# Kernel tuning notes

Measured on AMD Instinct MI355X. Metric: run time of the kernel, lower is better.

The kernel has to match this reference:

```python
import jax, jax.numpy as jnp
import numpy as np

B, N, E = 4, 8192, 131072
NODE_F, EDGE_F, HID, ACT = 16, 1, 128, 8


def _glorot(key, shape):
    fan_in, fan_out = shape[0], shape[1]
    lim = np.sqrt(6.0 / (fan_in + fan_out))
    return jax.random.uniform(key, shape, jnp.float32, -lim, lim)


def setup_inputs() -> dict:
    key = jax.random.key(0)
    ks = jax.random.split(key, 20)
    inp = {
        'node_features': jax.random.randint(ks[0], (B, N, NODE_F), 0, 10, jnp.int32),
        'edge_index': jax.random.randint(ks[1], (B, 2, E), 0, N, jnp.int64),
        'edge_features': jax.random.normal(ks[2], (B, E, EDGE_F), jnp.float32),
        # conv1: in = 2*NODE_F + EDGE_F
        'c1_w1': _glorot(ks[3], (2 * NODE_F + EDGE_F, HID)), 'c1_b1': jnp.zeros((HID,), jnp.float32),
        'c1_w2': _glorot(ks[4], (HID, HID)), 'c1_b2': jnp.zeros((HID,), jnp.float32),
        # conv2/conv3: in = 2*HID + 1
        'c2_w1': _glorot(ks[5], (2 * HID + 1, HID)), 'c2_b1': jnp.zeros((HID,), jnp.float32),
        'c2_w2': _glorot(ks[6], (HID, HID)), 'c2_b2': jnp.zeros((HID,), jnp.float32),
        'c3_w1': _glorot(ks[7], (2 * HID + 1, HID)), 'c3_b1': jnp.zeros((HID,), jnp.float32),
        'c3_w2': _glorot(ks[8], (HID, HID)), 'c3_b2': jnp.zeros((HID,), jnp.float32),
        'lin_w': _glorot(ks[9], (NODE_F + HID, ACT)), 'lin_b': jnp.zeros((ACT,), jnp.float32),
    }
    return inp


def _edge_conv(x, src, dst, ea, w1, b1, w2, b2):
    # message: cat([x_i (target), x_j (source), edge_attr]) -> Linear -> LeakyReLU -> Linear
    m = jnp.concatenate([x[dst], x[src], ea], axis=1)          # [E, 2F+EF]
    m = jax.nn.leaky_relu(m @ w1 + b1) @ w2 + b2               # [E, out]
    out = jax.ops.segment_min(m, dst, num_segments=x.shape[0])  # min-aggregate at targets
    cnt = jnp.zeros((x.shape[0],), m.dtype).at[dst].add(1.0)
    return jnp.where(cnt[:, None] > 0, out, 0.0)                # nodes w/o in-edges -> 0 (PyG)


def _graph_fwd(x0, ei, ea, p):
    x0 = x0.astype(jnp.float32)  # torch casts to IntTensor then MLP promotes; math on integer values
    src, dst = ei[0], ei[1]      # flow='source_to_target'
    x = jax.nn.leaky_relu(_edge_conv(x0, src, dst, ea, p['c1_w1'], p['c1_b1'], p['c1_w2'], p['c1_b2']))
    x = jax.nn.leaky_relu(_edge_conv(x, src, dst, ea, p['c2_w1'], p['c2_b1'], p['c2_w2'], p['c2_b2']))
    x = jax.nn.leaky_relu(_edge_conv(x, src, dst, ea, p['c3_w1'], p['c3_b1'], p['c3_w2'], p['c3_b2']))
    x = jnp.concatenate([x0, x], axis=1)
    return jax.nn.softplus(x @ p['lin_w'] + p['lin_b'])         # [N, ACT]


def reference(node_features, edge_index, edge_features,
              c1_w1, c1_b1, c1_w2, c1_b2,
              c2_w1, c2_b1, c2_w2, c2_b2,
              c3_w1, c3_b1, c3_w2, c3_b2,
              lin_w, lin_b):
    p = dict(c1_w1=c1_w1, c1_b1=c1_b1, c1_w2=c1_w2, c1_b2=c1_b2,
             c2_w1=c2_w1, c2_b1=c2_b1, c2_w2=c2_w2, c2_b2=c2_b2,
             c3_w1=c3_w1, c3_b1=c3_b1, c3_w2=c3_w2, c3_b2=c3_b2,
             lin_w=lin_w, lin_b=lin_b)
    return jax.vmap(lambda x, ei, ea: _graph_fwd(x, ei, ea, p))(
        node_features, edge_index, edge_features)               # [B, N, ACT]
```

## Files before the change

kernel.cpp:

```cpp
#include <hip/hip_runtime.h>

#define B_ 4
#define N_ 8192
#define E_ 131072
#define HID_ 128

typedef unsigned short us8 __attribute__((ext_vector_type(8)));
typedef unsigned short us4 __attribute__((ext_vector_type(4)));
typedef unsigned int   ui4 __attribute__((ext_vector_type(4)));
typedef int            i4  __attribute__((ext_vector_type(4)));
typedef __bf16         v8bf __attribute__((ext_vector_type(8)));
typedef float          v4f  __attribute__((ext_vector_type(4)));
typedef float          v2f  __attribute__((ext_vector_type(2)));

#define KEY_INF 0xFF800000u

__device__ __forceinline__ float b2f(unsigned short u) {
    return __uint_as_float(((unsigned)u) << 16);
}
__device__ __forceinline__ unsigned short f2b(float f) {
    unsigned x = __float_as_uint(f);
    return (unsigned short)((x + 0x7fffu + ((x >> 16) & 1u)) >> 16);
}
__device__ __forceinline__ unsigned fkey(float f) {
    unsigned b = __float_as_uint(f);
    return (b & 0x80000000u) ? ~b : (b | 0x80000000u);
}
__device__ __forceinline__ float funkey(unsigned k) {
    unsigned b = (k & 0x80000000u) ? (k ^ 0x80000000u) : ~k;
    return __uint_as_float(b);
}

__global__ void k_setup(const int* __restrict__ nf, unsigned short* __restrict__ x0b,
                        unsigned* __restrict__ cnt, unsigned* __restrict__ agg) {
    const int bid = blockIdx.x, tid = threadIdx.x;
    const int gid = bid * 256 + tid;
    ui4 v = {KEY_INF, KEY_INF, KEY_INF, KEY_INF};
    ((ui4*)agg)[gid] = v;
    if (bid < 512) {
        i4 x = ((const i4*)nf)[gid];
        us4 o;
        o[0] = f2b((float)x[0]); o[1] = f2b((float)x[1]);
        o[2] = f2b((float)x[2]); o[3] = f2b((float)x[3]);
        ((us4*)x0b)[gid] = o;
    }
    if (bid < 128) cnt[gid] = 0u;
}

__global__ void k_hist(const int* __restrict__ ei, unsigned* __restrict__ cnt) {
    int gid = blockIdx.x * 256 + threadIdx.x;
    int b = gid >> 17, e = gid & (E_ - 1);
    int dst = ei[(b << 18) + E_ + e];
    atomicAdd(&cnt[(b << 13) + dst], 1u);
}

__global__ void k_scan(unsigned* __restrict__ cnt) {
    int b = blockIdx.x;
    __shared__ unsigned ps[256];
    unsigned* c = cnt + (b << 13) + threadIdx.x * 32;
    unsigned loc[32]; unsigned s = 0;
#pragma unroll
    for (int i = 0; i < 32; i++) { loc[i] = c[i]; s += loc[i]; }
    ps[threadIdx.x] = s;
    __syncthreads();
    for (int off = 1; off < 256; off <<= 1) {
        unsigned v = (threadIdx.x >= (unsigned)off) ? ps[threadIdx.x - off] : 0u;
        __syncthreads();
        ps[threadIdx.x] += v;
        __syncthreads();
    }
    unsigned run = ps[threadIdx.x] - s;
#pragma unroll
    for (int i = 0; i < 32; i++) { c[i] = run; run += loc[i]; }
}

__global__ void k_scatter(const int* __restrict__ ei, unsigned* __restrict__ wptr,
                          int* __restrict__ perm) {
    int gid = blockIdx.x * 256 + threadIdx.x;
    int b = gid >> 17, e = gid & (E_ - 1);
    int dst = ei[(b << 18) + E_ + e];
    unsigned pos = atomicAdd(&wptr[(b << 13) + dst], 1u);
    perm[(b << 17) + pos] = e;
}

__device__ __forceinline__ void repack_one(const float* __restrict__ w1, const float* __restrict__ w2,
                                           unsigned short* __restrict__ w1n, unsigned short* __restrict__ w2t,
                                           int F, int KPAD, int gid) {
    int t1 = 256 * KPAD;
    if (gid < t1) {
        int j = gid / KPAD, k = gid - j * KPAD;
        float v = 0.f;
        if (k < F) v = (j < 128) ? w1[k * 128 + j] : w1[(F + k) * 128 + (j - 128)];
        w1n[gid] = f2b(v);
    } else {
        int g = gid - t1;
        if (g < 16384) { int j = g >> 7, k = g & 127; w2t[g] = f2b(w2[k * 128 + j]); }
    }
}

__global__ void k_repack3(const float* __restrict__ w1a, const float* __restrict__ w2a,
                          const float* __restrict__ w1b, const float* __restrict__ w2b,
                          const float* __restrict__ w1c, const float* __restrict__ w2c,
                          unsigned short* __restrict__ w1n0, unsigned short* __restrict__ w2t0,
                          unsigned short* __restrict__ w1n1, unsigned short* __restrict__ w2t1,
                          unsigned short* __restrict__ w1n2, unsigned short* __restrict__ w2t2) {
    const int bid = blockIdx.x;
    const int gid = bid * 256 + threadIdx.x;
    if (bid < 96)       repack_one(w1a, w2a, w1n0, w2t0, 16, 32, gid);
    else if (bid < 288) repack_one(w1b, w2b, w1n1, w2t1, 128, 128, gid - 96 * 256);
    else                repack_one(w1c, w2c, w1n2, w2t2, 128, 128, gid - 288 * 256);
}

template<int KPAD, bool FROM_AGG>
__global__ __launch_bounds__(256, 3) void k_node(
    const unsigned short* __restrict__ xin,
    unsigned* __restrict__ agg,
    const unsigned short* __restrict__ w1n,
    const float* __restrict__ bias1,
    unsigned short* __restrict__ Yd,
    unsigned short* __restrict__ Ys)
{
    constexpr int ASTR = KPAD + 8;
    __shared__ __align__(16) unsigned short A[64 * ASTR];
    __shared__ __align__(16) unsigned short Yb[64 * 264];

    const int tid = threadIdx.x;
    const int wave = tid >> 6, lane = tid & 63, lq = lane >> 4, lm = lane & 15;
    const int tile = (blockIdx.x & 7) * 64 + (blockIdx.x >> 3);
    const int n0 = tile * 64;

    v8bf wf[4][KPAD / 32]; float b1v[4];
#pragma unroll
    for (int nt = 0; nt < 4; nt++) {
        const int col = wave * 64 + nt * 16 + lm;
#pragma unroll
        for (int ks = 0; ks < KPAD / 32; ks++)
            wf[nt][ks] = *(const v8bf*)&w1n[col * KPAD + ks * 32 + lq * 8];
        b1v[nt] = (col < 128) ? bias1[col] : 0.f;
    }

    {
        const int row = tid >> 2, p = tid & 3;
        if (FROM_AGG) {
#pragma unroll
            for (int i = 0; i < 8; i++) {
                const int c = p + 4 * i;
                unsigned* ap = agg + ((size_t)(n0 + row)) * 128 + c * 4;
                ui4 k = *(ui4*)ap;
                ui4 inf = {KEY_INF, KEY_INF, KEY_INF, KEY_INF};
                *(ui4*)ap = inf;
                us4 o;
#pragma unroll
                for (int j = 0; j < 4; j++) {
                    float v = (k[j] == KEY_INF) ? 0.f : funkey(k[j]);
                    v = (v > 0.f) ? v : 0.01f * v;
                    o[j] = f2b(v);
                }
                *(us4*)&A[row * ASTR + c * 4] = o;
            }
        } else {
            us4 v = *(const us4*)(xin + ((size_t)(n0 + row)) * 16 + p * 4);
            *(us4*)&A[row * ASTR + p * 4] = v;
            us4 z = {0, 0, 0, 0};
            *(us4*)&A[row * ASTR + 16 + p * 4] = z;
        }
    }
    __syncthreads();

#pragma unroll
    for (int mt = 0; mt < 4; mt++) {
        v4f acc[4];
#pragma unroll
        for (int nt = 0; nt < 4; nt++) acc[nt] = v4f{0.f, 0.f, 0.f, 0.f};
#pragma unroll
        for (int ks = 0; ks < KPAD / 32; ks++) {
            v8bf a = *(const v8bf*)&A[(mt * 16 + lm) * ASTR + ks * 32 + lq * 8];
#pragma unroll
            for (int nt = 0; nt < 4; nt++)
                acc[nt] = __builtin_amdgcn_mfma_f32_16x16x32_bf16(a, wf[nt][ks], acc[nt], 0, 0, 0);
        }
#pragma unroll
        for (int nt = 0; nt < 4; nt++) {
            const int col = wave * 64 + nt * 16 + lm;
#pragma unroll
            for (int r = 0; r < 4; r++)
                Yb[(mt * 16 + lq * 4 + r) * 264 + col] = f2b(acc[nt][r] + b1v[nt]);
        }
    }
    __syncthreads();

    const int bb = tile >> 7, nl0 = (tile & 127) * 64;
#pragma unroll
    for (int i = 0; i < 8; i++) {
        const int idx = tid + 256 * i;
        const int row = idx >> 5, c = idx & 31;
        us8 v = *(const us8*)&Yb[row * 264 + c * 8];
        const int col0 = c * 8;
        unsigned short* dp = (col0 < 128)
            ? (Yd + ((size_t)(bb * N_) + nl0 + row) * 128 + col0)
            : (Ys + ((size_t)(bb * N_) + nl0 + row) * 128 + (col0 - 128));
        *(us8*)dp = v;
    }
}

__global__ __launch_bounds__(256, 4) void k_edge(
    const unsigned short* __restrict__ Yd,
    const unsigned short* __restrict__ Ys,
    const int* __restrict__ ei,
    const float* __restrict__ eaf,
    const int* __restrict__ perm,
    const unsigned short* __restrict__ w2t,
    const float* __restrict__ weap,
    const float* __restrict__ bias2,
    unsigned* __restrict__ agg)
{
    __shared__ __align__(16) unsigned short Hs[128 * 136];
    __shared__ __align__(16) int   dstl[128];
    __shared__ __align__(16) float weal[128];

    const int tid = threadIdx.x;
    const int wave = tid >> 6, lane = tid & 63, lq = lane >> 4, lm = lane & 15;

    if (tid < 128) weal[tid] = weap[tid];

    v8bf w2f[2][4]; float b2v[2];
#pragma unroll
    for (int nt = 0; nt < 2; nt++) {
        const int col = wave * 32 + nt * 16 + lm;
#pragma unroll
        for (int ks = 0; ks < 4; ks++)
            w2f[nt][ks] = *(const v8bf*)&w2t[col * 128 + ks * 32 + lq * 8];
        b2v[nt] = bias2[col];
    }
    __syncthreads();

    const int arow = tid >> 1, p = tid & 1;
    const int s = ((arow & 0x70) >> 2) | ((arow & 0x0C) << 3) | (arow & 3);

    int t = (blockIdx.x & 7) * 512 + (blockIdx.x >> 3);
    int b = t >> 10;
    int e = perm[(b << 17) + (t & 1023) * 128 + s];
    int src = ei[(b << 18) + e];
    int dst = ei[(b << 18) + E_ + e];
    float ea = eaf[(b << 17) + e];

    for (int jj = 0; jj < 4; jj++) {
        const int curb = b;
        if (p == 0) dstl[s] = dst;

        {
            const ui4* ydp = (const ui4*)(Yd + ((size_t)(curb * N_) + dst) * 128);
            const ui4* ysp = (const ui4*)(Ys + ((size_t)(curb * N_) + src) * 128);
            const v2f eav2 = {ea, ea};
            const v2f c01  = {0.01f, 0.01f};
            ui4 va = ydp[p], vb = ysp[p];
#pragma unroll
            for (int i = 0; i < 8; i++) {
                ui4 na, nb;
                if (i < 7) { na = ydp[p + 2 * (i + 1)]; nb = ysp[p + 2 * (i + 1)]; }
                const int c = p + 2 * i;
                ui4 od;
#pragma unroll
                for (int k = 0; k < 4; k++) {
                    v2f a, bb2, z, m;
                    a[0]   = __uint_as_float(va[k] << 16);
                    a[1]   = __uint_as_float(va[k] & 0xffff0000u);
                    bb2[0] = __uint_as_float(vb[k] << 16);
                    bb2[1] = __uint_as_float(vb[k] & 0xffff0000u);
                    v2f wv = *(const v2f*)&weal[c * 8 + 2 * k];
                    z = a + bb2 + wv * eav2;
                    m = z * c01;
                    float z0 = fmaxf(z[0], m[0]);
                    float z1 = fmaxf(z[1], m[1]);
                    od[k] = __builtin_amdgcn_perm(__float_as_uint(z1) + 0x8000u,
                                                  __float_as_uint(z0) + 0x8000u,
                                                  0x07060302u);
                }
                *(ui4*)&Hs[arow * 136 + c * 8] = od;
                va = na; vb = nb;
            }
        }
        __syncthreads();

        t += 128;
        if (jj < 3) {
            b = t >> 10;
            e = perm[(b << 17) + (t & 1023) * 128 + s];
            src = ei[(b << 18) + e];
            dst = ei[(b << 18) + E_ + e];
            ea = eaf[(b << 17) + e];
        }

        {
            const int col0 = wave * 32 + lm, col1 = col0 + 16;
            unsigned* aggb = agg + (size_t)(curb * N_) * 128;
            float cur0 = 0.f, cur1 = 0.f; int curd = -1;
#pragma unroll
            for (int mt = 0; mt < 8; mt++) {
                v4f acc0 = {0.f, 0.f, 0.f, 0.f}, acc1 = {0.f, 0.f, 0.f, 0.f};
#pragma unroll
                for (int ks = 0; ks < 4; ks++) {
                    v8bf a = *(const v8bf*)&Hs[(mt * 16 + lm) * 136 + ks * 32 + lq * 8];
                    acc0 = __builtin_amdgcn_mfma_f32_16x16x32_bf16(a, w2f[0][ks], acc0, 0, 0, 0);
                    acc1 = __builtin_amdgcn_mfma_f32_16x16x32_bf16(a, w2f[1][ks], acc1, 0, 0, 0);
                }
                i4 dv = *(const i4*)&dstl[lq * 32 + mt * 4];
#pragma unroll
                for (int r = 0; r < 4; r++) {
                    const float v0 = acc0[r] + b2v[0];
                    const float v1 = acc1[r] + b2v[1];
                    const int d = dv[r];
                    if (d != curd) {
                        if (curd >= 0) {
                            atomicMin(aggb + (size_t)curd * 128 + col0, fkey(cur0));
                            atomicMin(aggb + (size_t)curd * 128 + col1, fkey(cur1));
                        }
                        curd = d; cur0 = v0; cur1 = v1;
                    } else {
                        cur0 = fminf(cur0, v0); cur1 = fminf(cur1, v1);
                    }
                }
            }
            atomicMin(aggb + (size_t)curd * 128 + col0, fkey(cur0));
            atomicMin(aggb + (size_t)curd * 128 + col1, fkey(cur1));
        }
        __syncthreads();
    }
}

__global__ void k_final(const unsigned short* __restrict__ x0b, const unsigned* __restrict__ agg,
                        const float* __restrict__ lw, const float* __restrict__ lb,
                        float* __restrict__ out) {
    __shared__ float w[144 * 8];
    __shared__ float bias[8];
    for (int i = threadIdx.x; i < 1152; i += 256) w[i] = lw[i];
    if (threadIdx.x < 8) bias[threadIdx.x] = lb[threadIdx.x];
    __syncthreads();
    const int n = blockIdx.x * 256 + threadIdx.x;
    float acc[8];
#pragma unroll
    for (int a = 0; a < 8; a++) acc[a] = bias[a];
    const unsigned short* x0 = x0b + (size_t)n * 16;
#pragma unroll
    for (int f = 0; f < 16; f++) {
        const float xv = b2f(x0[f]);
#pragma unroll
        for (int a = 0; a < 8; a++) acc[a] += xv * w[f * 8 + a];
    }
    const unsigned* ar = agg + (size_t)n * 128;
    for (int f = 0; f < 128; f++) {
        const unsigned k = ar[f];
        float xv = (k == KEY_INF) ? 0.f : funkey(k);
        xv = (xv > 0.f) ? xv : 0.01f * xv;
#pragma unroll
        for (int a = 0; a < 8; a++) acc[a] += xv * w[(16 + f) * 8 + a];
    }
#pragma unroll
    for (int a = 0; a < 8; a++) {
        const float v = acc[a];
        const float sp = fmaxf(v, 0.f) + log1pf(expf(-fabsf(v)));
        out[(size_t)n * 8 + a] = sp;
    }
}

extern "C" void kernel_launch(void* const* d_in, const int* in_sizes, int n_in,
                              void* d_out, int out_size, void* d_ws, size_t ws_size,
                              hipStream_t stream) {
    (void)in_sizes; (void)n_in; (void)out_size; (void)ws_size;
    const int* nf  = (const int*)d_in[0];
    const int* ei  = (const int*)d_in[1];
    const float* eaf = (const float*)d_in[2];
    const float* cw1[3] = {(const float*)d_in[3],  (const float*)d_in[7],  (const float*)d_in[11]};
    const float* cb1[3] = {(const float*)d_in[4],  (const float*)d_in[8],  (const float*)d_in[12]};
    const float* cw2[3] = {(const float*)d_in[5],  (const float*)d_in[9],  (const float*)d_in[13]};
    const float* cb2[3] = {(const float*)d_in[6],  (const float*)d_in[10], (const float*)d_in[14]};
    const float* lw = (const float*)d_in[15];
    const float* lb = (const float*)d_in[16];
    float* out = (float*)d_out;

    size_t off = 0;
    auto carve = [&](size_t bytes) { void* p = (char*)d_ws + off; off += (bytes + 255) & ~(size_t)255; return p; };
    unsigned short* x0b  = (unsigned short*)carve((size_t)B_ * N_ * 16 * 2);
    unsigned*       agg  = (unsigned*)carve((size_t)B_ * N_ * 128 * 4);
    unsigned*       cnt  = (unsigned*)carve((size_t)B_ * N_ * 4);
    int*            perm = (int*)carve((size_t)B_ * E_ * 4);
    unsigned short* Yd   = (unsigned short*)carve((size_t)B_ * N_ * 128 * 2);
    unsigned short* Ys   = (unsigned short*)carve((size_t)B_ * N_ * 128 * 2);
    unsigned short* w1n0 = (unsigned short*)carve(256 * 32 * 2);
    unsigned short* w2t0 = (unsigned short*)carve(128 * 128 * 2);
    unsigned short* w1n1 = (unsigned short*)carve(256 * 128 * 2);
    unsigned short* w2t1 = (unsigned short*)carve(128 * 128 * 2);
    unsigned short* w1n2 = (unsigned short*)carve(256 * 128 * 2);
    unsigned short* w2t2 = (unsigned short*)carve(128 * 128 * 2);

    k_setup<<<4096, 256, 0, stream>>>(nf, x0b, cnt, agg);
    k_hist<<<2048, 256, 0, stream>>>(ei, cnt);
    k_scan<<<B_, 256, 0, stream>>>(cnt);
    k_scatter<<<2048, 256, 0, stream>>>(ei, cnt, perm);
    k_repack3<<<480, 256, 0, stream>>>(cw1[0], cw2[0], cw1[1], cw2[1], cw1[2], cw2[2],
                                       w1n0, w2t0, w1n1, w2t1, w1n2, w2t2);

    k_node<32, false><<<512, 256, 0, stream>>>(x0b, agg, w1n0, cb1[0], Yd, Ys);
    k_edge<<<1024, 256, 0, stream>>>(Yd, Ys, ei, eaf, perm, w2t0, cw1[0] + 32 * 128, cb2[0], agg);

    k_node<128, true><<<512, 256, 0, stream>>>(x0b, agg, w1n1, cb1[1], Yd, Ys);
    k_edge<<<1024, 256, 0, stream>>>(Yd, Ys, ei, eaf, perm, w2t1, cw1[1] + 256 * 128, cb2[1], agg);

    k_node<128, true><<<512, 256, 0, stream>>>(x0b, agg, w1n2, cb1[2], Yd, Ys);
    k_edge<<<1024, 256, 0, stream>>>(Yd, Ys, ei, eaf, perm, w2t2, cw1[2] + 256 * 128, cb2[2], agg);

    k_final<<<128, 256, 0, stream>>>(x0b, agg, lw, lb, out);
}
```

Measured before the change: 322.0 us.

## Halve edge tile to 64 rows for occupancy and restructure final kernel via LDS

The edge kernel now processes 64-edge tiles instead of 128, with four threads per row, half the LDS buffer and twice as many blocks. Launch bounds are raised to 8 waves per SIMD to increase occupancy and latency hiding for the gathers and atomics. The bias is folded into the MFMA accumulator init and leaky-relu uses a vector max. The final kernel stages decoded aggregates through LDS with coalesced loads and splits each node's 8 outputs over 4 threads, trading more blocks and register pressure for better memory coalescing.

```diff
diff --git a/kernel.cpp b/kernel.cpp
--- a/kernel.cpp
+++ b/kernel.cpp
@@ -203,7 +203,7 @@
     }
 }
 
-__global__ __launch_bounds__(256, 4) void k_edge(
+__global__ __launch_bounds__(256, 8) void k_edge(
     const unsigned short* __restrict__ Yd,
     const unsigned short* __restrict__ Ys,
     const int* __restrict__ ei,
@@ -214,8 +214,8 @@
     const float* __restrict__ bias2,
     unsigned* __restrict__ agg)
 {
-    __shared__ __align__(16) unsigned short Hs[128 * 136];
-    __shared__ __align__(16) int   dstl[128];
+    __shared__ __align__(16) unsigned short Hs[64 * 136];
+    __shared__ __align__(16) int   dstl[64];
     __shared__ __align__(16) float weal[128];
 
     const int tid = threadIdx.x;
@@ -234,12 +234,12 @@
     }
     __syncthreads();
 
-    const int arow = tid >> 1, p = tid & 1;
-    const int s = ((arow & 0x70) >> 2) | ((arow & 0x0C) << 3) | (arow & 3);
-
-    int t = (blockIdx.x & 7) * 512 + (blockIdx.x >> 3);
-    int b = t >> 10;
-    int e = perm[(b << 17) + (t & 1023) * 128 + s];
+    const int arow = tid >> 2, p = tid & 3;
+    const int s = ((arow & 0x0C) << 2) | ((arow >> 2) & 0x0C) | (arow & 3);
+
+    int t = (blockIdx.x & 7) * 1024 + (blockIdx.x >> 3);
+    int b = t >> 11;
+    int e = perm[(b << 17) + (t & 2047) * 64 + s];
     int src = ei[(b << 18) + e];
     int dst = ei[(b << 18) + E_ + e];
     float ea = eaf[(b << 17) + e];
@@ -255,25 +255,23 @@
             const v2f c01  = {0.01f, 0.01f};
             ui4 va = ydp[p], vb = ysp[p];
 #pragma unroll
-            for (int i = 0; i < 8; i++) {
+            for (int i = 0; i < 4; i++) {
                 ui4 na, nb;
-                if (i < 7) { na = ydp[p + 2 * (i + 1)]; nb = ysp[p + 2 * (i + 1)]; }
-                const int c = p + 2 * i;
+                if (i < 3) { na = ydp[p + 4 * (i + 1)]; nb = ysp[p + 4 * (i + 1)]; }
+                const int c = p + 4 * i;
                 ui4 od;
 #pragma unroll
                 for (int k = 0; k < 4; k++) {
-                    v2f a, bb2, z, m;
+                    v2f a, bb2, z;
                     a[0]   = __uint_as_float(va[k] << 16);
                     a[1]   = __uint_as_float(va[k] & 0xffff0000u);
                     bb2[0] = __uint_as_float(vb[k] << 16);
                     bb2[1] = __uint_as_float(vb[k] & 0xffff0000u);
                     v2f wv = *(const v2f*)&weal[c * 8 + 2 * k];
                     z = a + bb2 + wv * eav2;
-                    m = z * c01;
-                    float z0 = fmaxf(z[0], m[0]);
-                    float z1 = fmaxf(z[1], m[1]);
-                    od[k] = __builtin_amdgcn_perm(__float_as_uint(z1) + 0x8000u,
-                                                  __float_as_uint(z0) + 0x8000u,
+                    z = __builtin_elementwise_max(z, z * c01);
+                    od[k] = __builtin_amdgcn_perm(__float_as_uint(z[1]) + 0x8000u,
+                                                  __float_as_uint(z[0]) + 0x8000u,
                                                   0x07060302u);
                 }
                 *(ui4*)&Hs[arow * 136 + c * 8] = od;
@@ -282,10 +280,10 @@
         }
         __syncthreads();
 
-        t += 128;
+        t += 256;
         if (jj < 3) {
-            b = t >> 10;
-            e = perm[(b << 17) + (t & 1023) * 128 + s];
+            b = t >> 11;
+            e = perm[(b << 17) + (t & 2047) * 64 + s];
             src = ei[(b << 18) + e];
             dst = ei[(b << 18) + E_ + e];
             ea = eaf[(b << 17) + e];
@@ -296,19 +294,20 @@
             unsigned* aggb = agg + (size_t)(curb * N_) * 128;
             float cur0 = 0.f, cur1 = 0.f; int curd = -1;
 #pragma unroll
-            for (int mt = 0; mt < 8; mt++) {
-                v4f acc0 = {0.f, 0.f, 0.f, 0.f}, acc1 = {0.f, 0.f, 0.f, 0.f};
+            for (int mt = 0; mt < 4; mt++) {
+                v4f acc0 = {b2v[0], b2v[0], b2v[0], b2v[0]};
+                v4f acc1 = {b2v[1], b2v[1], b2v[1], b2v[1]};
 #pragma unroll
                 for (int ks = 0; ks < 4; ks++) {
                     v8bf a = *(const v8bf*)&Hs[(mt * 16 + lm) * 136 + ks * 32 + lq * 8];
                     acc0 = __builtin_amdgcn_mfma_f32_16x16x32_bf16(a, w2f[0][ks], acc0, 0, 0, 0);
                     acc1 = __builtin_amdgcn_mfma_f32_16x16x32_bf16(a, w2f[1][ks], acc1, 0, 0, 0);
                 }
-                i4 dv = *(const i4*)&dstl[lq * 32 + mt * 4];
+                i4 dv = *(const i4*)&dstl[lq * 16 + mt * 4];
 #pragma unroll
                 for (int r = 0; r < 4; r++) {
-                    const float v0 = acc0[r] + b2v[0];
-                    const float v1 = acc1[r] + b2v[1];
+                    const float v0 = acc0[r];
+                    const float v1 = acc1[r];
                     const int d = dv[r];
                     if (d != curd) {
                         if (curd >= 0) {
@@ -328,39 +327,48 @@
     }
 }
 
-__global__ void k_final(const unsigned short* __restrict__ x0b, const unsigned* __restrict__ agg,
-                        const float* __restrict__ lw, const float* __restrict__ lb,
-                        float* __restrict__ out) {
+__global__ __launch_bounds__(256, 4) void k_final(
+    const unsigned short* __restrict__ x0b, const unsigned* __restrict__ agg,
+    const float* __restrict__ lw, const float* __restrict__ lb,
+    float* __restrict__ out) {
     __shared__ float w[144 * 8];
-    __shared__ float bias[8];
-    for (int i = threadIdx.x; i < 1152; i += 256) w[i] = lw[i];
-    if (threadIdx.x < 8) bias[threadIdx.x] = lb[threadIdx.x];
+    __shared__ float bias8[8];
+    __shared__ float xs[64 * 129];
+    const int tid = threadIdx.x;
+    for (int i = tid; i < 1152; i += 256) w[i] = lw[i];
+    if (tid < 8) bias8[tid] = lb[tid];
+    const int n0 = blockIdx.x * 64;
+#pragma unroll
+    for (int i = 0; i < 8; i++) {
+        const int idx = tid + 256 * i;
+        const int row = idx >> 5, c = idx & 31;
+        ui4 k = ((const ui4*)(agg + ((size_t)(n0 + row)) * 128))[c];
+#pragma unroll
+        for (int j = 0; j < 4; j++) {
+            float v = (k[j] == KEY_INF) ? 0.f : funkey(k[j]);
+            v = fmaxf(v, 0.01f * v);
+            xs[row * 129 + c * 4 + j] = v;
+        }
+    }
     __syncthreads();
-    const int n = blockIdx.x * 256 + threadIdx.x;
-    float acc[8];
-#pragma unroll
-    for (int a = 0; a < 8; a++) acc[a] = bias[a];
-    const unsigned short* x0 = x0b + (size_t)n * 16;
+    const int node = tid >> 2, ap = (tid & 3) * 2;
+    float a0 = bias8[ap], a1 = bias8[ap + 1];
+    const unsigned short* x0 = x0b + (size_t)(n0 + node) * 16;
 #pragma unroll
     for (int f = 0; f < 16; f++) {
         const float xv = b2f(x0[f]);
-#pragma unroll
-        for (int a = 0; a < 8; a++) acc[a] += xv * w[f * 8 + a];
-    }
-    const unsigned* ar = agg + (size_t)n * 128;
+        a0 += xv * w[f * 8 + ap]; a1 += xv * w[f * 8 + ap + 1];
+    }
+    const float* xr = &xs[node * 129];
+#pragma unroll 8
     for (int f = 0; f < 128; f++) {
-        const unsigned k = ar[f];
-        float xv = (k == KEY_INF) ? 0.f : funkey(k);
-        xv = (xv > 0.f) ? xv : 0.01f * xv;
-#pragma unroll
-        for (int a = 0; a < 8; a++) acc[a] += xv * w[(16 + f) * 8 + a];
-    }
-#pragma unroll
-    for (int a = 0; a < 8; a++) {
-        const float v = acc[a];
-        const float sp = fmaxf(v, 0.f) + log1pf(expf(-fabsf(v)));
-        out[(size_t)n * 8 + a] = sp;
-    }
+        const float xv = xr[f];
+        a0 += xv * w[(16 + f) * 8 + ap]; a1 += xv * w[(16 + f) * 8 + ap + 1];
+    }
+    v2f o;
+    o[0] = fmaxf(a0, 0.f) + log1pf(expf(-fabsf(a0)));
+    o[1] = fmaxf(a1, 0.f) + log1pf(expf(-fabsf(a1)));
+    *(v2f*)&out[(size_t)(n0 + node) * 8 + ap] = o;
 }
 
 extern "C" void kernel_launch(void* const* d_in, const int* in_sizes, int n_in,
@@ -401,13 +409,13 @@
                                        w1n0, w2t0, w1n1, w2t1, w1n2, w2t2);
 
     k_node<32, false><<<512, 256, 0, stream>>>(x0b, agg, w1n0, cb1[0], Yd, Ys);
-    k_edge<<<1024, 256, 0, stream>>>(Yd, Ys, ei, eaf, perm, w2t0, cw1[0] + 32 * 128, cb2[0], agg);
+    k_edge<<<2048, 256, 0, stream>>>(Yd, Ys, ei, eaf, perm, w2t0, cw1[0] + 32 * 128, cb2[0], agg);
 
     k_node<128, true><<<512, 256, 0, stream>>>(x0b, agg, w1n1, cb1[1], Yd, Ys);
-    k_edge<<<1024, 256, 0, stream>>>(Yd, Ys, ei, eaf, perm, w2t1, cw1[1] + 256 * 128, cb2[1], agg);
+    k_edge<<<2048, 256, 0, stream>>>(Yd, Ys, ei, eaf, perm, w2t1, cw1[1] + 256 * 128, cb2[1], agg);
 
     k_node<128, true><<<512, 256, 0, stream>>>(x0b, agg, w1n2, cb1[2], Yd, Ys);
-    k_edge<<<1024, 256, 0, stream>>>(Yd, Ys, ei, eaf, perm, w2t2, cw1[2] + 256 * 128, cb2[2], agg);
-
-    k_final<<<128, 256, 0, stream>>>(x0b, agg, lw, lb, out);
-}
+    k_edge<<<2048, 256, 0, stream>>>(Yd, Ys, ei, eaf, perm, w2t2, cw1[2] + 256 * 128, cb2[2], agg);
+
+    k_final<<<512, 256, 0, stream>>>(x0b, agg, lw, lb, out);
+}
```

Result: slower. 571.5 us (+77.5%).
